# Performance work log

Hardware: AMD Instinct MI355X
Metric: run time of the kernel (lower is better)

Reference implementation:

```python
import jax, jax.numpy as jnp
import numpy as np

BATCH = 32768
D = 1024          # vector dimension
BITS = 4          # total bit budget
MSE_BITS = BITS - 1
K = 2 ** MSE_BITS # 8 codebook centroids
QJL_DIM = D       # default qjl projection dim


def setup_inputs() -> dict:
    key = jax.random.key(0)
    kx, kq, ks = jax.random.split(key, 3)
    x = jax.random.normal(kx, (BATCH, D), dtype=jnp.float32)
    # Haar-random rotation: QR of Gaussian with sign-fixed R diagonal
    G = jax.random.normal(kq, (D, D), dtype=jnp.float32)
    Q, R = jnp.linalg.qr(G)
    s = jnp.sign(jnp.diag(R))
    s = jnp.where(s == 0, 1.0, s)
    Pi = Q * s[None, :]
    # QJL projection matrix S: iid N(0,1), shape (m, d)
    S = jax.random.normal(ks, (QJL_DIM, D), dtype=jnp.float32)
    # Lloyd-Max-style scalar codebook for N(0,1): Gaussian quantile centroids
    probs = (jnp.arange(K, dtype=jnp.float32) + 0.5) / K
    centroids = (jnp.sqrt(2.0) * jax.scipy.special.erfinv(2.0 * probs - 1.0)).astype(jnp.float32)
    return {"x": x, "Pi": Pi, "centroids": centroids, "S": S}


def reference(x, Pi, centroids, S):
    # Stage 1 (MSE quantizer): rotate, per-coordinate nearest-centroid, gather, unrotate
    y = x @ Pi.T                                   # (B, D)
    diffs = jnp.abs(y[..., None] - centroids)      # (B, D, K)
    mse_indices = jnp.argmin(diffs, axis=-1)       # (B, D) int
    y_hat = centroids[mse_indices]                 # (B, D)
    x_hat = y_hat @ Pi                             # (B, D)
    # Stage 2 (QJL on residual)
    residual = x - x_hat                           # (B, D)
    residual_norm = jnp.linalg.norm(residual, axis=-1)  # (B,)
    projected = residual @ S.T                     # (B, m)
    qjl_signs = jnp.sign(projected)
    qjl_signs = jnp.where(qjl_signs == 0, 1.0, qjl_signs)
    return mse_indices, qjl_signs, residual_norm
```

## Files before the change

### kernel.cpp

```cpp
#include <hip/hip_runtime.h>
#include <math.h>

#define B_ROWS 32768
#define DIM    1024
#define PADA   268
#define PADB   140


struct FragT { float4 a[8]; float4 b[4]; };

__device__ __forceinline__ void loadT(const float* pA, const float* pB, FragT& f) {
#pragma unroll
    for (int i = 0; i < 8; ++i) f.a[i] = *(const float4*)(pA + (size_t)(32 * i) * DIM);
#pragma unroll
    for (int i = 0; i < 4; ++i) f.b[i] = *(const float4*)(pB + (size_t)(32 * i) * DIM);
}

__device__ __forceinline__ void storeT(const FragT& f, float (*As)[PADA], float (*Bs)[PADB],
                                       int kq, int r0) {
    const int c0 = kq * 4, sh = 4 * (kq >> 1);
#pragma unroll
    for (int i = 0; i < 8; ++i) {
        const int col = r0 + 32 * i + sh;
        As[c0 + 0][col] = f.a[i].x; As[c0 + 1][col] = f.a[i].y;
        As[c0 + 2][col] = f.a[i].z; As[c0 + 3][col] = f.a[i].w;
    }
#pragma unroll
    for (int i = 0; i < 4; ++i) {
        const int col = r0 + 32 * i + sh;
        Bs[c0 + 0][col] = f.b[i].x; Bs[c0 + 1][col] = f.b[i].y;
        Bs[c0 + 2][col] = f.b[i].z; Bs[c0 + 3][col] = f.b[i].w;
    }
}

__device__ __forceinline__ void compute16x8(const float (*As)[PADA], const float (*Bs)[PADB],
                                            int tx, int ty, float (&acc)[16][8]) {
#pragma unroll
    for (int kk = 0; kk < 32; ++kk) {
        const int sh = 4 * (kk >> 3);
        const float4 A0 = *(const float4*)&As[kk][4 * ty + sh];
        const float4 A1 = *(const float4*)&As[kk][4 * ty + 64 + sh];
        const float4 A2 = *(const float4*)&As[kk][4 * ty + 128 + sh];
        const float4 A3 = *(const float4*)&As[kk][4 * ty + 192 + sh];
        const float4 B0 = *(const float4*)&Bs[kk][4 * tx + sh];
        const float4 B1 = *(const float4*)&Bs[kk][4 * tx + 64 + sh];
        const float a[16] = {A0.x, A0.y, A0.z, A0.w, A1.x, A1.y, A1.z, A1.w,
                             A2.x, A2.y, A2.z, A2.w, A3.x, A3.y, A3.z, A3.w};
        const float b[8]  = {B0.x, B0.y, B0.z, B0.w, B1.x, B1.y, B1.z, B1.w};
#pragma unroll
        for (int i = 0; i < 16; ++i)
#pragma unroll
            for (int j = 0; j < 8; ++j)
                acc[i][j] = fmaf(a[i], b[j], acc[i][j]);
    }
}

__device__ __forceinline__ void runT(const float* Ab, const float* Bb, int m0, int n0,
                                     int koff, int tid,
                                     float (*As)[PADA], float (*Bs)[PADB],
                                     float (&acc)[16][8]) {
    const int tx = tid & 15, ty = tid >> 4, kq = tid & 7, r0 = tid >> 3;
    const float* pA = Ab + (size_t)(m0 + r0) * DIM + koff + kq * 4;
    const float* pB = Bb + (size_t)(n0 + r0) * DIM + koff + kq * 4;
    FragT f;
    loadT(pA, pB, f);
    for (int t = 0; t < 16; ++t) {
        __syncthreads();
        storeT(f, As, Bs, kq, r0);
        __syncthreads();
        if (t < 15) loadT(pA + (t + 1) * 32, pB + (t + 1) * 32, f);
        compute16x8(As, Bs, tx, ty, acc);
    }
}

__device__ __forceinline__ void runG(const unsigned char* idxb, const float* Pi,
                                     const float* clut, int m0, int n0, int koff, int tid,
                                     float (*As)[PADA], float (*Bs)[PADB],
                                     float (&acc)[16][8]) {
    const int tx = tid & 15, ty = tid >> 4, kq = tid & 7, r0 = tid >> 3;
    const int nq = tid & 31, kr0 = tid >> 5;
    const unsigned char* pA = idxb + (size_t)(m0 + r0) * DIM + koff + kq * 4;
    const float*         pB = Pi + (size_t)(koff + kr0) * DIM + n0 + nq * 4;
    uchar4 ka[8]; float4 kb[4];
#pragma unroll
    for (int i = 0; i < 8; ++i) ka[i] = *(const uchar4*)(pA + (size_t)(32 * i) * DIM);
#pragma unroll
    for (int i = 0; i < 4; ++i) kb[i] = *(const float4*)(pB + (size_t)(8 * i) * DIM);
    for (int t = 0; t < 16; ++t) {
        __syncthreads();
        {
            const int c0 = kq * 4, sh = 4 * (kq >> 1);
#pragma unroll
            for (int i = 0; i < 8; ++i) {
                const int col = r0 + 32 * i + sh;
                As[c0 + 0][col] = clut[ka[i].x]; As[c0 + 1][col] = clut[ka[i].y];
                As[c0 + 2][col] = clut[ka[i].z]; As[c0 + 3][col] = clut[ka[i].w];
            }
#pragma unroll
            for (int i = 0; i < 4; ++i)
                *(float4*)&Bs[kr0 + 8 * i][nq * 4 + 4 * i] = kb[i];
        }
        __syncthreads();
        if (t < 15) {
#pragma unroll
            for (int i = 0; i < 8; ++i)
                ka[i] = *(const uchar4*)(pA + (t + 1) * 32 + (size_t)(32 * i) * DIM);
#pragma unroll
            for (int i = 0; i < 4; ++i)
                kb[i] = *(const float4*)(pB + (size_t)((t + 1) * 32 + 8 * i) * DIM);
        }
        compute16x8(As, Bs, tx, ty, acc);
    }
}

__global__ __launch_bounds__(256) void kT_part(
    const float* __restrict__ A, const float* __restrict__ B, float* __restrict__ part)
{
    __shared__ float As[32][PADA];
    __shared__ float Bs[32][PADB];
    const int tid = threadIdx.x, tx = tid & 15, ty = tid >> 4;
    const int m0 = blockIdx.y * 256, n0 = blockIdx.x * 128;
    float acc[16][8] = {};
    runT(A, B, m0, n0, 0, tid, As, Bs, acc);
#pragma unroll
    for (int i = 0; i < 16; ++i) {
        const int row = m0 + 64 * (i >> 2) + 4 * ty + (i & 3);
        const size_t o = (size_t)row * DIM + n0 + tx * 4;
        *(float4*)&part[o]      = make_float4(acc[i][0], acc[i][1], acc[i][2], acc[i][3]);
        *(float4*)&part[o + 64] = make_float4(acc[i][4], acc[i][5], acc[i][6], acc[i][7]);
    }
}

__global__ __launch_bounds__(256) void k1_final(
    const float* __restrict__ X, const float* __restrict__ Pi, const float* __restrict__ C,
    const float* __restrict__ part, float* __restrict__ idxf, unsigned char* __restrict__ idx8)
{
    __shared__ float As[32][PADA];
    __shared__ float Bs[32][PADB];
    const int tid = threadIdx.x, tx = tid & 15, ty = tid >> 4;
    const int m0 = blockIdx.y * 256, n0 = blockIdx.x * 128;
    float acc[16][8] = {};
    runT(X, Pi, m0, n0, 512, tid, As, Bs, acc);
    float c8[8];
#pragma unroll
    for (int t = 0; t < 8; ++t) c8[t] = C[t];
#pragma unroll
    for (int i = 0; i < 16; ++i) {
        const int row = m0 + 64 * (i >> 2) + 4 * ty + (i & 3);
        const size_t o = (size_t)row * DIM + n0 + tx * 4;
        const float4 p1l = *(const float4*)&part[o];
        const float4 p1h = *(const float4*)&part[o + 64];
        const float y[8] = {p1l.x + acc[i][0], p1l.y + acc[i][1], p1l.z + acc[i][2], p1l.w + acc[i][3],
                            p1h.x + acc[i][4], p1h.y + acc[i][5], p1h.z + acc[i][6], p1h.w + acc[i][7]};
        float fv[8]; unsigned char bv[8];
#pragma unroll
        for (int j = 0; j < 8; ++j) {
            float best = fabsf(y[j] - c8[0]); int bi = 0;
#pragma unroll
            for (int t2 = 1; t2 < 8; ++t2) {
                const float d = fabsf(y[j] - c8[t2]);
                if (d < best) { best = d; bi = t2; }
            }
            fv[j] = (float)bi; bv[j] = (unsigned char)bi;
        }
        *(float4*)&idxf[o]      = make_float4(fv[0], fv[1], fv[2], fv[3]);
        *(float4*)&idxf[o + 64] = make_float4(fv[4], fv[5], fv[6], fv[7]);
        *(uchar4*)&idx8[o]      = make_uchar4(bv[0], bv[1], bv[2], bv[3]);
        *(uchar4*)&idx8[o + 64] = make_uchar4(bv[4], bv[5], bv[6], bv[7]);
    }
}

__global__ __launch_bounds__(256) void k3_part(
    const unsigned char* __restrict__ idx8, const float* __restrict__ Pi,
    const float* __restrict__ C, float* __restrict__ part)
{
    __shared__ float As[32][PADA];
    __shared__ float Bs[32][PADB];
    __shared__ float clut[8];
    const int tid = threadIdx.x, tx = tid & 15, ty = tid >> 4;
    const int m0 = blockIdx.y * 256, n0 = blockIdx.x * 128;
    if (tid < 8) clut[tid] = C[tid];
    float acc[16][8] = {};
    runG(idx8, Pi, clut, m0, n0, 0, tid, As, Bs, acc);
#pragma unroll
    for (int i = 0; i < 16; ++i) {
        const int row = m0 + 64 * (i >> 2) + 4 * ty + (i & 3);
        const size_t o = (size_t)row * DIM + n0 + tx * 4;
        *(float4*)&part[o]      = make_float4(acc[i][0], acc[i][1], acc[i][2], acc[i][3]);
        *(float4*)&part[o + 64] = make_float4(acc[i][4], acc[i][5], acc[i][6], acc[i][7]);
    }
}

__global__ __launch_bounds__(256) void k3_final(
    const float* __restrict__ X, const float* __restrict__ Pi, const float* __restrict__ C,
    const unsigned char* __restrict__ idx8, const float* __restrict__ part,
    float* __restrict__ R, double* __restrict__ nrm2)
{
    __shared__ float As[32][PADA];
    __shared__ float Bs[32][PADB];
    __shared__ float clut[8];
    const int tid = threadIdx.x, tx = tid & 15, ty = tid >> 4;
    const int m0 = blockIdx.y * 256, n0 = blockIdx.x * 128;
    if (tid < 8) clut[tid] = C[tid];
    float acc[16][8] = {};
    runG(idx8, Pi, clut, m0, n0, 512, tid, As, Bs, acc);
#pragma unroll
    for (int i = 0; i < 16; ++i) {
        const int row = m0 + 64 * (i >> 2) + 4 * ty + (i & 3);
        const size_t o = (size_t)row * DIM + n0 + tx * 4;
        const float4 p1l = *(const float4*)&part[o];
        const float4 p1h = *(const float4*)&part[o + 64];
        const float4 x0 = *(const float4*)&X[o];
        const float4 x1 = *(const float4*)&X[o + 64];
        float rv[8];
        rv[0] = x0.x - (p1l.x + acc[i][0]); rv[1] = x0.y - (p1l.y + acc[i][1]);
        rv[2] = x0.z - (p1l.z + acc[i][2]); rv[3] = x0.w - (p1l.w + acc[i][3]);
        rv[4] = x1.x - (p1h.x + acc[i][4]); rv[5] = x1.y - (p1h.y + acc[i][5]);
        rv[6] = x1.z - (p1h.z + acc[i][6]); rv[7] = x1.w - (p1h.w + acc[i][7]);
        *(float4*)&R[o]      = make_float4(rv[0], rv[1], rv[2], rv[3]);
        *(float4*)&R[o + 64] = make_float4(rv[4], rv[5], rv[6], rv[7]);
        double s = 0.0;
#pragma unroll
        for (int j = 0; j < 8; ++j) s = fma((double)rv[j], (double)rv[j], s);
#pragma unroll
        for (int mask = 1; mask < 16; mask <<= 1) s += __shfl_xor(s, mask, 16);
        if (tx == 0) atomicAdd(&nrm2[row], s);
    }
}

__global__ __launch_bounds__(256) void k5_final(
    const float* __restrict__ R, const float* __restrict__ S, float* psgn)
{
    __shared__ float As[32][PADA];
    __shared__ float Bs[32][PADB];
    const int tid = threadIdx.x, tx = tid & 15, ty = tid >> 4;
    const int m0 = blockIdx.y * 256, n0 = blockIdx.x * 128;
    float acc[16][8] = {};
    runT(R, S, m0, n0, 512, tid, As, Bs, acc);
#pragma unroll
    for (int i = 0; i < 16; ++i) {
        const int row = m0 + 64 * (i >> 2) + 4 * ty + (i & 3);
        const size_t o = (size_t)row * DIM + n0 + tx * 4;
        const float4 p1l = *(const float4*)&psgn[o];
        const float4 p1h = *(const float4*)&psgn[o + 64];
        const float p[8] = {p1l.x + acc[i][0], p1l.y + acc[i][1], p1l.z + acc[i][2], p1l.w + acc[i][3],
                            p1h.x + acc[i][4], p1h.y + acc[i][5], p1h.z + acc[i][6], p1h.w + acc[i][7]};
        *(float4*)&psgn[o]      = make_float4((p[0] >= 0.f) ? 1.f : -1.f, (p[1] >= 0.f) ? 1.f : -1.f,
                                              (p[2] >= 0.f) ? 1.f : -1.f, (p[3] >= 0.f) ? 1.f : -1.f);
        *(float4*)&psgn[o + 64] = make_float4((p[4] >= 0.f) ? 1.f : -1.f, (p[5] >= 0.f) ? 1.f : -1.f,
                                              (p[6] >= 0.f) ? 1.f : -1.f, (p[7] >= 0.f) ? 1.f : -1.f);
    }
}

__global__ __launch_bounds__(256) void kN_sqrt(const double* __restrict__ nrm2, float* __restrict__ nrm)
{
    const int i = blockIdx.x * 256 + threadIdx.x;
    if (i < B_ROWS) nrm[i] = (float)sqrt(nrm2[i]);
}

extern "C" void kernel_launch(void* const* d_in, const int* in_sizes, int n_in,
                              void* d_out, int out_size, void* d_ws, size_t ws_size,
                              hipStream_t stream) {
    const float* X  = (const float*)d_in[0];
    const float* Pi = (const float*)d_in[1];
    const float* C  = (const float*)d_in[2];
    const float* S  = (const float*)d_in[3];

    float* out  = (float*)d_out;
    float* idxf = out;
    float* sgn  = out + (size_t)B_ROWS * DIM;
    float* nrm  = sgn + (size_t)B_ROWS * DIM;

    char* ws = (char*)d_ws;
    float*         R    = (float*)ws;
    unsigned char* idx8 = (unsigned char*)(ws + (size_t)B_ROWS * DIM * 4);
    double*        nrm2 = (double*)(ws + (size_t)B_ROWS * DIM * 5);

    hipMemsetAsync(nrm2, 0, (size_t)B_ROWS * sizeof(double), stream);

    dim3 blk(256);
    dim3 gG(DIM / 128, B_ROWS / 256);

    kT_part <<<gG, blk, 0, stream>>>(X, Pi, sgn);
    k1_final<<<gG, blk, 0, stream>>>(X, Pi, C, sgn, idxf, idx8);
    k3_part <<<gG, blk, 0, stream>>>(idx8, Pi, C, sgn);
    k3_final<<<gG, blk, 0, stream>>>(X, Pi, C, idx8, sgn, R, nrm2);
    kN_sqrt <<<dim3(B_ROWS / 256), blk, 0, stream>>>(nrm2, nrm);
    kT_part <<<gG, blk, 0, stream>>>(R, S, sgn);
    k5_final<<<gG, blk, 0, stream>>>(R, S, sgn);
}
```

Baseline: 2.852 ms.

## Double-buffer LDS tiles with 16-wide K chunks in all GEMM kernels

```diff
diff --git a/kernel.cpp b/kernel.cpp
--- a/kernel.cpp
+++ b/kernel.cpp
@@ -7,36 +7,37 @@
 #define PADB   140
 
 
-struct FragT { float4 a[8]; float4 b[4]; };
-
-__device__ __forceinline__ void loadT(const float* pA, const float* pB, FragT& f) {
-#pragma unroll
-    for (int i = 0; i < 8; ++i) f.a[i] = *(const float4*)(pA + (size_t)(32 * i) * DIM);
-#pragma unroll
-    for (int i = 0; i < 4; ++i) f.b[i] = *(const float4*)(pB + (size_t)(32 * i) * DIM);
-}
-
-__device__ __forceinline__ void storeT(const FragT& f, float (*As)[PADA], float (*Bs)[PADB],
-                                       int kq, int r0) {
+struct Frag16  { float4 a[4]; float4 b[2]; };
+struct FragG16 { uchar4 a[4]; float4 b[2]; };
+
+__device__ __forceinline__ void load16(const float* pA, const float* pB, Frag16& f) {
+#pragma unroll
+    for (int i = 0; i < 4; ++i) f.a[i] = *(const float4*)(pA + (size_t)(64 * i) * DIM);
+#pragma unroll
+    for (int i = 0; i < 2; ++i) f.b[i] = *(const float4*)(pB + (size_t)(64 * i) * DIM);
+}
+
+__device__ __forceinline__ void store16(const Frag16& f, float (*As)[PADA], float (*Bs)[PADB],
+                                        int kq, int r) {
     const int c0 = kq * 4, sh = 4 * (kq >> 1);
 #pragma unroll
-    for (int i = 0; i < 8; ++i) {
-        const int col = r0 + 32 * i + sh;
+    for (int i = 0; i < 4; ++i) {
+        const int col = r + 64 * i + sh;
         As[c0 + 0][col] = f.a[i].x; As[c0 + 1][col] = f.a[i].y;
         As[c0 + 2][col] = f.a[i].z; As[c0 + 3][col] = f.a[i].w;
     }
 #pragma unroll
-    for (int i = 0; i < 4; ++i) {
-        const int col = r0 + 32 * i + sh;
+    for (int i = 0; i < 2; ++i) {
+        const int col = r + 64 * i + sh;
         Bs[c0 + 0][col] = f.b[i].x; Bs[c0 + 1][col] = f.b[i].y;
         Bs[c0 + 2][col] = f.b[i].z; Bs[c0 + 3][col] = f.b[i].w;
     }
 }
 
-__device__ __forceinline__ void compute16x8(const float (*As)[PADA], const float (*Bs)[PADB],
-                                            int tx, int ty, float (&acc)[16][8]) {
-#pragma unroll
-    for (int kk = 0; kk < 32; ++kk) {
+__device__ __forceinline__ void compute16(const float (*As)[PADA], const float (*Bs)[PADB],
+                                          int tx, int ty, float (&acc)[16][8]) {
+#pragma unroll
+    for (int kk = 0; kk < 16; ++kk) {
         const int sh = 4 * (kk >> 3);
         const float4 A0 = *(const float4*)&As[kk][4 * ty + sh];
         const float4 A1 = *(const float4*)&As[kk][4 * ty + 64 + sh];
@@ -55,73 +56,86 @@
     }
 }
 
-__device__ __forceinline__ void runT(const float* Ab, const float* Bb, int m0, int n0,
-                                     int koff, int tid,
-                                     float (*As)[PADA], float (*Bs)[PADB],
-                                     float (&acc)[16][8]) {
-    const int tx = tid & 15, ty = tid >> 4, kq = tid & 7, r0 = tid >> 3;
-    const float* pA = Ab + (size_t)(m0 + r0) * DIM + koff + kq * 4;
-    const float* pB = Bb + (size_t)(n0 + r0) * DIM + koff + kq * 4;
-    FragT f;
-    loadT(pA, pB, f);
-    for (int t = 0; t < 16; ++t) {
+__device__ __forceinline__ void runT16(const float* Ab, const float* Bb, int m0, int n0,
+                                       int koff, int tid,
+                                       float (*As0)[PADA], float (*Bs0)[PADB],
+                                       float (*As1)[PADA], float (*Bs1)[PADB],
+                                       float (&acc)[16][8]) {
+    const int tx = tid & 15, ty = tid >> 4, kq = tid & 3, r = tid >> 2;
+    const float* pA = Ab + (size_t)(m0 + r) * DIM + koff + kq * 4;
+    const float* pB = Bb + (size_t)(n0 + r) * DIM + koff + kq * 4;
+    Frag16 f;
+    load16(pA, pB, f);
+    store16(f, As0, Bs0, kq, r);
+    for (int c = 0; c < 32; c += 2) {
         __syncthreads();
-        storeT(f, As, Bs, kq, r0);
+        load16(pA + (c + 1) * 16, pB + (c + 1) * 16, f);
+        compute16(As0, Bs0, tx, ty, acc);
+        store16(f, As1, Bs1, kq, r);
         __syncthreads();
-        if (t < 15) loadT(pA + (t + 1) * 32, pB + (t + 1) * 32, f);
-        compute16x8(As, Bs, tx, ty, acc);
-    }
-}
-
-__device__ __forceinline__ void runG(const unsigned char* idxb, const float* Pi,
-                                     const float* clut, int m0, int n0, int koff, int tid,
-                                     float (*As)[PADA], float (*Bs)[PADB],
-                                     float (&acc)[16][8]) {
-    const int tx = tid & 15, ty = tid >> 4, kq = tid & 7, r0 = tid >> 3;
-    const int nq = tid & 31, kr0 = tid >> 5;
-    const unsigned char* pA = idxb + (size_t)(m0 + r0) * DIM + koff + kq * 4;
-    const float*         pB = Pi + (size_t)(koff + kr0) * DIM + n0 + nq * 4;
-    uchar4 ka[8]; float4 kb[4];
-#pragma unroll
-    for (int i = 0; i < 8; ++i) ka[i] = *(const uchar4*)(pA + (size_t)(32 * i) * DIM);
-#pragma unroll
-    for (int i = 0; i < 4; ++i) kb[i] = *(const float4*)(pB + (size_t)(8 * i) * DIM);
-    for (int t = 0; t < 16; ++t) {
+        if (c < 30) load16(pA + (c + 2) * 16, pB + (c + 2) * 16, f);
+        compute16(As1, Bs1, tx, ty, acc);
+        if (c < 30) store16(f, As0, Bs0, kq, r);
+    }
+}
+
+__device__ __forceinline__ void runG16(const unsigned char* idxb, const float* Pi,
+                                       const float* clut, int m0, int n0, int koff, int tid,
+                                       float (*As0)[PADA], float (*Bs0)[PADB],
+                                       float (*As1)[PADA], float (*Bs1)[PADB],
+                                       float (&acc)[16][8]) {
+    const int tx = tid & 15, ty = tid >> 4, kq = tid & 3, r = tid >> 2;
+    const int nq = tid & 31, kr = tid >> 5;
+    const unsigned char* pA = idxb + (size_t)(m0 + r) * DIM + koff + kq * 4;
+    const float*         pB = Pi + (size_t)(koff + kr) * DIM + n0 + nq * 4;
+    FragG16 f;
+#pragma unroll
+    for (int i = 0; i < 4; ++i) f.a[i] = *(const uchar4*)(pA + (size_t)(64 * i) * DIM);
+#pragma unroll
+    for (int i = 0; i < 2; ++i) f.b[i] = *(const float4*)(pB + (size_t)(8 * i) * DIM);
+#define STORE_G(As, Bs)                                                          \
+    {   const int c0 = kq * 4, sh = 4 * (kq >> 1);                               \
+        _Pragma("unroll")                                                        \
+        for (int i = 0; i < 4; ++i) {                                            \
+            const int col = r + 64 * i + sh;                                     \
+            As[c0 + 0][col] = clut[f.a[i].x]; As[c0 + 1][col] = clut[f.a[i].y];  \
+            As[c0 + 2][col] = clut[f.a[i].z]; As[c0 + 3][col] = clut[f.a[i].w];  \
+        }                                                                        \
+        _Pragma("unroll")                                                        \
+        for (int i = 0; i < 2; ++i)                                              \
+            *(float4*)&Bs[kr + 8 * i][nq * 4 + 4 * i] = f.b[i];                  \
+    }
+#define LOAD_G(cc)                                                               \
+    {   _Pragma("unroll")                                                        \
+        for (int i = 0; i < 4; ++i)                                              \
+            f.a[i] = *(const uchar4*)(pA + (cc) * 16 + (size_t)(64 * i) * DIM);  \
+        _Pragma("unroll")                                                        \
+        for (int i = 0; i < 2; ++i)                                              \
+            f.b[i] = *(const float4*)(pB + (size_t)((cc) * 16 + 8 * i) * DIM);   \
+    }
+    STORE_G(As0, Bs0);
+    for (int c = 0; c < 32; c += 2) {
         __syncthreads();
-        {
-            const int c0 = kq * 4, sh = 4 * (kq >> 1);
-#pragma unroll
-            for (int i = 0; i < 8; ++i) {
-                const int col = r0 + 32 * i + sh;
-                As[c0 + 0][col] = clut[ka[i].x]; As[c0 + 1][col] = clut[ka[i].y];
-                As[c0 + 2][col] = clut[ka[i].z]; As[c0 + 3][col] = clut[ka[i].w];
-            }
-#pragma unroll
-            for (int i = 0; i < 4; ++i)
-                *(float4*)&Bs[kr0 + 8 * i][nq * 4 + 4 * i] = kb[i];
-        }
+        LOAD_G(c + 1);
+        compute16(As0, Bs0, tx, ty, acc);
+        STORE_G(As1, Bs1);
         __syncthreads();
-        if (t < 15) {
-#pragma unroll
-            for (int i = 0; i < 8; ++i)
-                ka[i] = *(const uchar4*)(pA + (t + 1) * 32 + (size_t)(32 * i) * DIM);
-#pragma unroll
-            for (int i = 0; i < 4; ++i)
-                kb[i] = *(const float4*)(pB + (size_t)((t + 1) * 32 + 8 * i) * DIM);
-        }
-        compute16x8(As, Bs, tx, ty, acc);
-    }
+        if (c < 30) LOAD_G(c + 2);
+        compute16(As1, Bs1, tx, ty, acc);
+        if (c < 30) STORE_G(As0, Bs0);
+    }
+#undef STORE_G
+#undef LOAD_G
 }
 
 __global__ __launch_bounds__(256) void kT_part(
     const float* __restrict__ A, const float* __restrict__ B, float* __restrict__ part)
 {
-    __shared__ float As[32][PADA];
-    __shared__ float Bs[32][PADB];
-    const int tid = threadIdx.x, tx = tid & 15, ty = tid >> 4;
-    const int m0 = blockIdx.y * 256, n0 = blockIdx.x * 128;
-    float acc[16][8] = {};
-    runT(A, B, m0, n0, 0, tid, As, Bs, acc);
+    __shared__ float As0[16][PADA], Bs0[16][PADB], As1[16][PADA], Bs1[16][PADB];
+    const int tid = threadIdx.x, tx = tid & 15, ty = tid >> 4;
+    const int m0 = blockIdx.y * 256, n0 = blockIdx.x * 128;
+    float acc[16][8] = {};
+    runT16(A, B, m0, n0, 0, tid, As0, Bs0, As1, Bs1, acc);
 #pragma unroll
     for (int i = 0; i < 16; ++i) {
         const int row = m0 + 64 * (i >> 2) + 4 * ty + (i & 3);
@@ -135,12 +149,11 @@
     const float* __restrict__ X, const float* __restrict__ Pi, const float* __restrict__ C,
     const float* __restrict__ part, float* __restrict__ idxf, unsigned char* __restrict__ idx8)
 {
-    __shared__ float As[32][PADA];
-    __shared__ float Bs[32][PADB];
-    const int tid = threadIdx.x, tx = tid & 15, ty = tid >> 4;
-    const int m0 = blockIdx.y * 256, n0 = blockIdx.x * 128;
-    float acc[16][8] = {};
-    runT(X, Pi, m0, n0, 512, tid, As, Bs, acc);
+    __shared__ float As0[16][PADA], Bs0[16][PADB], As1[16][PADA], Bs1[16][PADB];
+    const int tid = threadIdx.x, tx = tid & 15, ty = tid >> 4;
+    const int m0 = blockIdx.y * 256, n0 = blockIdx.x * 128;
+    float acc[16][8] = {};
+    runT16(X, Pi, m0, n0, 512, tid, As0, Bs0, As1, Bs1, acc);
     float c8[8];
 #pragma unroll
     for (int t = 0; t < 8; ++t) c8[t] = C[t];
@@ -174,14 +187,14 @@
     const unsigned char* __restrict__ idx8, const float* __restrict__ Pi,
     const float* __restrict__ C, float* __restrict__ part)
 {
-    __shared__ float As[32][PADA];
-    __shared__ float Bs[32][PADB];
+    __shared__ float As0[16][PADA], Bs0[16][PADB], As1[16][PADA], Bs1[16][PADB];
     __shared__ float clut[8];
     const int tid = threadIdx.x, tx = tid & 15, ty = tid >> 4;
     const int m0 = blockIdx.y * 256, n0 = blockIdx.x * 128;
     if (tid < 8) clut[tid] = C[tid];
-    float acc[16][8] = {};
-    runG(idx8, Pi, clut, m0, n0, 0, tid, As, Bs, acc);
+    __syncthreads();
+    float acc[16][8] = {};
+    runG16(idx8, Pi, clut, m0, n0, 0, tid, As0, Bs0, As1, Bs1, acc);
 #pragma unroll
     for (int i = 0; i < 16; ++i) {
         const int row = m0 + 64 * (i >> 2) + 4 * ty + (i & 3);
@@ -196,14 +209,14 @@
     const unsigned char* __restrict__ idx8, const float* __restrict__ part,
     float* __restrict__ R, double* __restrict__ nrm2)
 {
-    __shared__ float As[32][PADA];
-    __shared__ float Bs[32][PADB];
+    __shared__ float As0[16][PADA], Bs0[16][PADB], As1[16][PADA], Bs1[16][PADB];
     __shared__ float clut[8];
     const int tid = threadIdx.x, tx = tid & 15, ty = tid >> 4;
     const int m0 = blockIdx.y * 256, n0 = blockIdx.x * 128;
     if (tid < 8) clut[tid] = C[tid];
-    float acc[16][8] = {};
-    runG(idx8, Pi, clut, m0, n0, 512, tid, As, Bs, acc);
+    __syncthreads();
+    float acc[16][8] = {};
+    runG16(idx8, Pi, clut, m0, n0, 512, tid, As0, Bs0, As1, Bs1, acc);
 #pragma unroll
     for (int i = 0; i < 16; ++i) {
         const int row = m0 + 64 * (i >> 2) + 4 * ty + (i & 3);
@@ -231,12 +244,11 @@
 __global__ __launch_bounds__(256) void k5_final(
     const float* __restrict__ R, const float* __restrict__ S, float* psgn)
 {
-    __shared__ float As[32][PADA];
-    __shared__ float Bs[32][PADB];
-    const int tid = threadIdx.x, tx = tid & 15, ty = tid >> 4;
-    const int m0 = blockIdx.y * 256, n0 = blockIdx.x * 128;
-    float acc[16][8] = {};
-    runT(R, S, m0, n0, 512, tid, As, Bs, acc);
+    __shared__ float As0[16][PADA], Bs0[16][PADB], As1[16][PADA], Bs1[16][PADB];
+    const int tid = threadIdx.x, tx = tid & 15, ty = tid >> 4;
+    const int m0 = blockIdx.y * 256, n0 = blockIdx.x * 128;
+    float acc[16][8] = {};
+    runT16(R, S, m0, n0, 512, tid, As0, Bs0, As1, Bs1, acc);
 #pragma unroll
     for (int i = 0; i < 16; ++i) {
         const int row = m0 + 64 * (i >> 2) + 4 * ty + (i & 3);
```

Measured after the change: 5.449 ms. +91.1%, slower.
